# Kernel optimization log

Hardware: AMD Instinct MI355X
Metric: run time of the kernel (lower is better)

Reference implementation:

```python
import jax, jax.numpy as jnp
import numpy as np

NUM_HEADS = 8


def setup_inputs() -> dict:
    key = jax.random.key(0)
    ks = jax.random.split(key, 6)
    B, S, H = 2, 4096, 512
    Q = jax.random.normal(ks[0], (B, S, H), dtype=jnp.float32)
    K = jax.random.normal(ks[1], (B, S, H), dtype=jnp.float32)
    V = jax.random.normal(ks[2], (B, S, H), dtype=jnp.float32)
    risk_sigma = jax.random.uniform(ks[3], (B, 1), dtype=jnp.float32) * 0.2
    risk_lambda = jnp.array([2.0], dtype=jnp.float32)
    W_out = jax.random.normal(ks[4], (H, H), dtype=jnp.float32) * (1.0 / np.sqrt(H))
    b_out = jnp.zeros((H,), dtype=jnp.float32)
    return {"Q": Q, "K": K, "V": V, "risk_sigma": risk_sigma,
            "risk_lambda": risk_lambda, "W_out": W_out, "b_out": b_out}


def reference(Q, K, V, risk_sigma, risk_lambda, W_out, b_out):
    B, S, H = Q.shape
    nh = NUM_HEADS
    hd = H // nh
    # split heads: [B, S, nh, hd]
    q = Q.reshape(B, S, nh, hd)
    k = K.reshape(B, S, nh, hd)
    v = V.reshape(B, S, nh, hd)
    scale = 1.0 / jnp.sqrt(jnp.asarray(hd, dtype=Q.dtype))
    # [B, nh, S, S]
    scores = jnp.einsum('bshd,bthd->bhst', q, k) * scale
    # distance-based risk penalty
    pos = jnp.arange(S, dtype=Q.dtype)
    norm_dist = jnp.abs(pos[None, :] - pos[:, None]) / S  # [S, S]
    dist_sq = norm_dist ** 2
    sigma_c = jnp.clip(risk_sigma, 0.001, 0.2)            # [B, 1]
    sigma_n = (sigma_c - 0.001) / (0.2 - 0.001)
    lam = (risk_lambda / 10.0).reshape(())                 # scalar
    risk_term = lam * sigma_n[:, :, None, None] * dist_sq[None, None]  # [B,1,S,S]
    attn = jax.nn.softmax(scores - risk_term, axis=-1)
    ctx = jnp.einsum('bhst,bthd->bshd', attn, v).reshape(B, S, H)
    return ctx @ W_out.T + b_out
```

## Files before the change

kernel.cpp:

```cpp
#include <hip/hip_runtime.h>
#include <hip/hip_bf16.h>


#define S_LEN 4096
#define NHEAD 8
#define HD 64
#define HTOT 512

typedef __attribute__((ext_vector_type(8))) short short8;
typedef __attribute__((ext_vector_type(4))) float floatx4;
typedef __attribute__((ext_vector_type(2))) _Float16 half2v;

#if __has_builtin(__builtin_amdgcn_exp2f)
#define EXP2F(x) __builtin_amdgcn_exp2f(x)
#else
#define EXP2F(x) exp2f(x)
#endif

__device__ __forceinline__ unsigned pack_bf16(float a, float b) {
    unsigned ua = __builtin_bit_cast(unsigned, a) + 0x8000u;
    unsigned ub = __builtin_bit_cast(unsigned, b) + 0x8000u;
    return __builtin_amdgcn_perm(ub, ua, 0x07060302u);
}

__device__ __forceinline__ unsigned short f2bf(float x) {
    unsigned u = __builtin_bit_cast(unsigned, x) + 0x8000u;
    return (unsigned short)(u >> 16);
}

__device__ __forceinline__ void async16(const unsigned short* g, unsigned short* l) {
    __builtin_amdgcn_global_load_lds(
        (const __attribute__((address_space(1))) unsigned int*)g,
        (__attribute__((address_space(3))) unsigned int*)l, 16, 0, 0);
}

__global__ __launch_bounds__(256) void prep_kernel(
    const float* __restrict__ K, unsigned short* __restrict__ K16,
    const float* __restrict__ V, unsigned short* __restrict__ Vt,
    const float* __restrict__ W, unsigned short* __restrict__ W16)
{
    const int tid = threadIdx.x;
    if (blockIdx.x >= 3072) {
        size_t i = ((size_t)(blockIdx.x - 3072) * 256 + tid) * 8;
        float4 a = *(const float4*)(W + i);
        float4 b = *(const float4*)(W + i + 4);
        unsigned o[4] = {pack_bf16(a.x, a.y), pack_bf16(a.z, a.w),
                         pack_bf16(b.x, b.y), pack_bf16(b.z, b.w)};
        *(short8*)(W16 + i) = *(short8*)o;
    } else if (blockIdx.x < 2048) {
        size_t i = ((size_t)blockIdx.x * 256 + tid) * 8;
        float4 a = *(const float4*)(K + i);
        float4 b = *(const float4*)(K + i + 4);
        unsigned o[4] = {pack_bf16(a.x, a.y), pack_bf16(a.z, a.w),
                         pack_bf16(b.x, b.y), pack_bf16(b.z, b.w)};
        *(short8*)(K16 + i) = *(short8*)o;
    } else {
        __shared__ unsigned short T[64 * 66];
        const int blk = blockIdx.x - 2048;
        const int st = blk & 63;
        const int bh = blk >> 6;
        const int b = bh >> 3, h = bh & 7;
        const float* src = V + ((size_t)b * S_LEN + st * 64) * HTOT + h * HD;
        for (int i = 0; i < 4; i++) {
            int idx = tid + i * 256;
            int s = idx >> 4, c4 = idx & 15;
            float4 v = *(const float4*)(src + (size_t)s * HTOT + c4 * 4);
            T[(c4 * 4 + 0) * 66 + s] = f2bf(v.x);
            T[(c4 * 4 + 1) * 66 + s] = f2bf(v.y);
            T[(c4 * 4 + 2) * 66 + s] = f2bf(v.z);
            T[(c4 * 4 + 3) * 66 + s] = f2bf(v.w);
        }
        __syncthreads();
        unsigned short* dst = Vt + ((size_t)bh * 64) * S_LEN + st * 64;
        for (int i = 0; i < 2; i++) {
            int idx = tid + i * 256;
            int d = idx >> 3, c8 = idx & 7;
            uint2 lo = *(const uint2*)&T[d * 66 + c8 * 8];
            uint2 hi = *(const uint2*)&T[d * 66 + c8 * 8 + 4];
            unsigned o[4] = {lo.x, lo.y, hi.x, hi.y};
            *(short8*)(dst + (size_t)d * S_LEN + c8 * 8) = *(short8*)o;
        }
    }
}

__global__ __launch_bounds__(256, 4) void attn_kernel(
    const float* __restrict__ Q, const unsigned short* __restrict__ K16,
    const unsigned short* __restrict__ Vt,
    const float* __restrict__ risk_sigma, const float* __restrict__ risk_lambda,
    _Float16* __restrict__ Cpart, float* __restrict__ Lpart)
{
    __shared__ unsigned short Ksh[2][64 * 64];
    __shared__ unsigned short Vsh[2][64 * 64];

    const int tid  = threadIdx.x;
    const int wave = tid >> 6;
    const int lane = tid & 63;
    const int quad = lane >> 4;
    const int ln   = lane & 15;
    const int sw   = ln & 7;

    const int bid = blockIdx.x;
    const int ks  = bid & 1;
    const int qt  = (bid >> 1) & 31;
    const int h   = (bid >> 6) & 7;
    const int b   = bid >> 9;
    const int qbase = qt * 128;

    float sig = risk_sigma[b];
    sig = fminf(fmaxf(sig, 0.001f), 0.2f);
    const float sn   = (sig - 0.001f) * (1.0f / 0.199f);
    const float coef = risk_lambda[0] * 0.1f * sn;
    const float nc2 = -coef * (1.0f / 4096.0f) * (1.0f / 4096.0f) * 1.4426950408889634f;
    const float qscale = 0.125f * 1.4426950408889634f;

    const float* Qb = Q + (size_t)b * S_LEN * HTOT + (size_t)h * HD;
    const unsigned short* Kb = K16 + (size_t)b * S_LEN * HTOT + (size_t)h * HD;
    const unsigned short* Vb = Vt + ((size_t)(b * 8 + h) * 64) * S_LEN;

    const int rl  = lane >> 3;
    const int c8g = ((lane & 7) ^ rl) << 3;
    const int ksrow = ((wave & 1) << 4) | (((rl >> 2) & 1) << 3)
                    | ((wave >> 1) << 2) | (rl & 3);

    auto dma = [&](int buf, int kb) {
        const unsigned short* gv = Vb + (size_t)(wave * 8 + rl) * S_LEN + kb + c8g;
        async16(Kb + (size_t)(kb + ksrow) * HTOT + c8g,
                &Ksh[buf][wave * 512 + lane * 8]);
        async16(Kb + (size_t)(kb + 32 + ksrow) * HTOT + c8g,
                &Ksh[buf][(wave + 4) * 512 + lane * 8]);
        async16(gv,              &Vsh[buf][wave * 512 + lane * 8]);
        async16(gv + 32 * S_LEN, &Vsh[buf][(wave + 4) * 512 + lane * 8]);
    };

    dma(0, ks * 2048);

    short8 qf[2][2];
    {
        const float* qp0 = Qb + (size_t)(qbase + wave * 32 + ln) * HTOT + quad * 8;
        #pragma unroll
        for (int nt = 0; nt < 2; nt++) {
            const float* qp = qp0 + (size_t)(nt * 16) * HTOT;
            #pragma unroll
            for (int half = 0; half < 2; half++) {
                float4 x = *(const float4*)(qp + half * 32);
                float4 y = *(const float4*)(qp + half * 32 + 4);
                unsigned o[4] = {pack_bf16(x.x * qscale, x.y * qscale),
                                 pack_bf16(x.z * qscale, x.w * qscale),
                                 pack_bf16(y.x * qscale, y.y * qscale),
                                 pack_bf16(y.z * qscale, y.w * qscale)};
                qf[nt][half] = *(short8*)o;
            }
        }
    }
    __syncthreads();

    const short sone = (short)0x3F80;
    const short8 ones = {sone, sone, sone, sone, sone, sone, sone, sone};

    floatx4 Oacc[2][4], Lacc[2];
    #pragma unroll
    for (int nt = 0; nt < 2; nt++) {
        Lacc[nt] = (floatx4){0.f, 0.f, 0.f, 0.f};
        #pragma unroll
        for (int dt = 0; dt < 4; dt++) Oacc[nt][dt] = (floatx4){0.f, 0.f, 0.f, 0.f};
    }

    const int qa = qbase + wave * 32;
    const float quad8f = (float)(quad * 8);

    for (int kt = 0; kt < 32; ++kt) {
        const int kbase = ks * 2048 + kt * 64;
        const int cur = kt & 1;
        if (kt < 31) dma(1 - cur, kbase + 64);
        const unsigned short* Kc = Ksh[cur];
        const unsigned short* Vc = Vsh[cur];

        const float dqq = (float)(qa + ln - kbase) - quad8f;
        unsigned pw[2][2][4];

        #pragma unroll
        for (int jt = 0; jt < 4; jt++) {
            const int krow = (jt * 16 + ln) * 64;
            short8 ak0 = *(const short8*)&Kc[krow + ((quad ^ sw) << 3)];
            short8 ak1 = *(const short8*)&Kc[krow + (((quad + 4) ^ sw) << 3)];
            const float jtoff = (float)((jt >> 1) * 32 + (jt & 1) * 4);
            #pragma unroll
            for (int nt = 0; nt < 2; nt++) {
                float d = dqq + ((float)(nt * 16) - jtoff);
                floatx4 rk;
                #pragma unroll
                for (int r = 0; r < 4; r++) {
                    rk[r] = (nc2 * d) * d;
                    d -= 1.0f;
                }
                floatx4 s = __builtin_amdgcn_mfma_f32_16x16x32_bf16(ak0, qf[nt][0], rk, 0, 0, 0);
                s = __builtin_amdgcn_mfma_f32_16x16x32_bf16(ak1, qf[nt][1], s, 0, 0, 0);
                float p0 = EXP2F(s[0]);
                float p1 = EXP2F(s[1]);
                float p2 = EXP2F(s[2]);
                float p3 = EXP2F(s[3]);
                pw[nt][jt >> 1][(jt & 1) * 2 + 0] = pack_bf16(p0, p1);
                pw[nt][jt >> 1][(jt & 1) * 2 + 1] = pack_bf16(p2, p3);
            }
        }

        __builtin_amdgcn_s_setprio(1);
        #pragma unroll
        for (int dt = 0; dt < 4; dt++) {
            const int vrow = (dt * 16 + ln) * 64;
            short8 bv0 = *(const short8*)&Vc[vrow + ((quad ^ sw) << 3)];
            short8 bv1 = *(const short8*)&Vc[vrow + (((quad + 4) ^ sw) << 3)];
            #pragma unroll
            for (int nt = 0; nt < 2; nt++) {
                short8 pa0 = *(const short8*)&pw[nt][0][0];
                short8 pa1 = *(const short8*)&pw[nt][1][0];
                Oacc[nt][dt] = __builtin_amdgcn_mfma_f32_16x16x32_bf16(pa0, bv0, Oacc[nt][dt], 0, 0, 0);
                Oacc[nt][dt] = __builtin_amdgcn_mfma_f32_16x16x32_bf16(pa1, bv1, Oacc[nt][dt], 0, 0, 0);
            }
        }
        #pragma unroll
        for (int nt = 0; nt < 2; nt++) {
            short8 pa0 = *(const short8*)&pw[nt][0][0];
            short8 pa1 = *(const short8*)&pw[nt][1][0];
            Lacc[nt] = __builtin_amdgcn_mfma_f32_16x16x32_bf16(pa0, ones, Lacc[nt], 0, 0, 0);
            Lacc[nt] = __builtin_amdgcn_mfma_f32_16x16x32_bf16(pa1, ones, Lacc[nt], 0, 0, 0);
        }
        __builtin_amdgcn_s_setprio(0);
        __syncthreads();
    }

    _Float16* Cw = Cpart + (size_t)bid * (128 * 64);
    for (int nt = 0; nt < 2; nt++) {
        if (ln == 0) {
            #pragma unroll
            for (int r = 0; r < 4; r++)
                Lpart[bid * 128 + wave * 32 + nt * 16 + quad * 4 + r] = Lacc[nt][r];
        }
        float rl4[4];
        #pragma unroll
        for (int r = 0; r < 4; r++) rl4[r] = 1.0f / Lacc[nt][r];
        for (int dt = 0; dt < 4; dt++)
            #pragma unroll
            for (int r = 0; r < 4; r++) {
                int q = wave * 32 + nt * 16 + quad * 4 + r;
                Cw[q * 64 + dt * 16 + ln] = (_Float16)(Oacc[nt][dt][r] * rl4[r]);
            }
    }
}

__global__ __launch_bounds__(256) void combine_kernel(
    const _Float16* __restrict__ Cpart, const float* __restrict__ Lpart,
    unsigned short* __restrict__ ctx)
{
    const int t = threadIdx.x;
    const int tile = blockIdx.x;
    const int qt = tile & 31, h = (tile >> 5) & 7, b = tile >> 8;
    __shared__ float w0s[128], w1s[128];
    if (t < 128) {
        float l0 = Lpart[(tile * 2 + 0) * 128 + t];
        float l1 = Lpart[(tile * 2 + 1) * 128 + t];
        float inv = 1.0f / (l0 + l1);
        w0s[t] = l0 * inv;
        w1s[t] = l1 * inv;
    }
    __syncthreads();
    const _Float16* C0 = Cpart + (size_t)(tile * 2) * (128 * 64);
    const _Float16* C1 = C0 + 128 * 64;
    for (int i = 0; i < 8; i++) {
        int e = (i * 256 + t) * 4;
        int q = e >> 6, d = e & 63;
        half2v a0 = *(const half2v*)(C0 + e);
        half2v a1 = *(const half2v*)(C0 + e + 2);
        half2v b0 = *(const half2v*)(C1 + e);
        half2v b1 = *(const half2v*)(C1 + e + 2);
        float w0 = w0s[q], w1 = w1s[q];
        float v0 = w0 * (float)a0[0] + w1 * (float)b0[0];
        float v1 = w0 * (float)a0[1] + w1 * (float)b0[1];
        float v2 = w0 * (float)a1[0] + w1 * (float)b1[0];
        float v3 = w0 * (float)a1[1] + w1 * (float)b1[1];
        uint2 o;
        o.x = pack_bf16(v0, v1);
        o.y = pack_bf16(v2, v3);
        *(uint2*)&ctx[((size_t)b * S_LEN + qt * 128 + q) * HTOT + h * HD + d] = o;
    }
}

__global__ __launch_bounds__(256) void proj_kernel(
    const unsigned short* __restrict__ A,
    const unsigned short* __restrict__ W16,
    const float* __restrict__ bias,
    float* __restrict__ out)
{
    __shared__ unsigned short Ash[2][64 * 32];
    __shared__ unsigned short Bsh[2][128 * 32];
    const int tid = threadIdx.x;
    const int wave = tid >> 6, lane = tid & 63, quad = lane >> 4, ln = lane & 15;
    const int wr = wave >> 1, wc = wave & 1;
    const int m0 = blockIdx.y * 64;
    const int nb = blockIdx.x * 128;

    const int arow = (wave * 64 + lane) >> 2;
    const int ac   = (wave * 64 + lane) & 3;
    const int acs  = (ac ^ ((arow >> 1) & 3)) << 3;
    const int wrow0 = (wave * 64 + lane) >> 2;
    const int wc0   = (wave * 64 + lane) & 3;
    const int wcs0  = (wc0 ^ ((wrow0 >> 1) & 3)) << 3;
    const int wrow1 = wrow0 + 64;
    const int wcs1  = (wc0 ^ ((wrow1 >> 1) & 3)) << 3;

    auto dma = [&](int buf, int k0) {
        async16(A + (size_t)(m0 + arow) * 512 + k0 + acs,
                &Ash[buf][wave * 512 + lane * 8]);
        async16(W16 + (size_t)(nb + wrow0) * 512 + k0 + wcs0,
                &Bsh[buf][wave * 512 + lane * 8]);
        async16(W16 + (size_t)(nb + wrow1) * 512 + k0 + wcs1,
                &Bsh[buf][(wave + 4) * 512 + lane * 8]);
    };

    floatx4 acc[2][4];
    for (int i = 0; i < 2; i++)
        for (int j = 0; j < 4; j++) acc[i][j] = (floatx4){0.f, 0.f, 0.f, 0.f};

    dma(0, 0);
    for (int kt = 0; kt < 16; ++kt) {
        const int cur = kt & 1;
        __syncthreads();
        if (kt < 15) dma(1 - cur, (kt + 1) * 32);

        short8 af[2], bf[4];
        for (int i = 0; i < 2; i++) {
            int r = wr * 32 + i * 16 + ln;
            af[i] = *(const short8*)&Ash[cur][r * 32 + ((quad ^ ((r >> 1) & 3)) << 3)];
        }
        for (int j = 0; j < 4; j++) {
            int r = wc * 64 + j * 16 + ln;
            bf[j] = *(const short8*)&Bsh[cur][r * 32 + ((quad ^ ((r >> 1) & 3)) << 3)];
        }
        for (int i = 0; i < 2; i++)
            for (int j = 0; j < 4; j++)
                acc[i][j] = __builtin_amdgcn_mfma_f32_16x16x32_bf16(af[i], bf[j], acc[i][j], 0, 0, 0);
    }

    for (int i = 0; i < 2; i++) {
        int row = m0 + wr * 32 + i * 16 + quad * 4;
        for (int j = 0; j < 4; j++) {
            int col = nb + wc * 64 + j * 16 + ln;
            float bv = bias[col];
            #pragma unroll
            for (int r = 0; r < 4; r++)
                out[(size_t)(row + r) * 512 + col] = acc[i][j][r] + bv;
        }
    }
}

extern "C" void kernel_launch(void* const* d_in, const int* in_sizes, int n_in,
                              void* d_out, int out_size, void* d_ws, size_t ws_size,
                              hipStream_t stream) {
    const float* Q    = (const float*)d_in[0];
    const float* K    = (const float*)d_in[1];
    const float* V    = (const float*)d_in[2];
    const float* sig  = (const float*)d_in[3];
    const float* lam  = (const float*)d_in[4];
    const float* W    = (const float*)d_in[5];
    const float* bias = (const float*)d_in[6];

    unsigned short* K16 = (unsigned short*)d_ws;
    unsigned short* Vt  = (unsigned short*)((char*)d_ws + (8u << 20));
    unsigned short* ctx = (unsigned short*)((char*)d_ws + (16u << 20));
    float* Lpart        = (float*)((char*)d_ws + (24u << 20));
    unsigned short* W16 = (unsigned short*)((char*)d_ws + (24u << 20) + (512u << 10));
    _Float16* Cpart     = (_Float16*)d_out;
    float* out = (float*)d_out;

    prep_kernel<<<dim3(3200), dim3(256), 0, stream>>>(K, K16, V, Vt, W, W16);
    attn_kernel<<<dim3(1024), dim3(256), 0, stream>>>(Q, K16, Vt, sig, lam, Cpart, Lpart);
    combine_kernel<<<dim3(512), dim3(256), 0, stream>>>(Cpart, Lpart, ctx);
    proj_kernel<<<dim3(4, 128), dim3(256), 0, stream>>>(ctx, W16, bias, out);
}
```

Baseline: 205.8 us.

## Fuse split-K combine into attention block using two wave groups

After: 201.3 us. -2.2%, faster.

```diff
diff --git a/kernel.cpp b/kernel.cpp
--- a/kernel.cpp
+++ b/kernel.cpp
@@ -9,7 +9,6 @@
 
 typedef __attribute__((ext_vector_type(8))) short short8;
 typedef __attribute__((ext_vector_type(4))) float floatx4;
-typedef __attribute__((ext_vector_type(2))) _Float16 half2v;
 
 #if __has_builtin(__builtin_amdgcn_exp2f)
 #define EXP2F(x) __builtin_amdgcn_exp2f(x)
@@ -83,27 +82,27 @@
     }
 }
 
-__global__ __launch_bounds__(256, 4) void attn_kernel(
+__global__ __launch_bounds__(512, 4) void attn_kernel(
     const float* __restrict__ Q, const unsigned short* __restrict__ K16,
     const unsigned short* __restrict__ Vt,
     const float* __restrict__ risk_sigma, const float* __restrict__ risk_lambda,
-    _Float16* __restrict__ Cpart, float* __restrict__ Lpart)
+    unsigned short* __restrict__ ctx)
 {
-    __shared__ unsigned short Ksh[2][64 * 64];
-    __shared__ unsigned short Vsh[2][64 * 64];
+    __shared__ unsigned short SH[32768];
 
     const int tid  = threadIdx.x;
     const int wave = tid >> 6;
+    const int grp  = wave >> 2;
+    const int wv   = wave & 3;
     const int lane = tid & 63;
     const int quad = lane >> 4;
     const int ln   = lane & 15;
     const int sw   = ln & 7;
 
     const int bid = blockIdx.x;
-    const int ks  = bid & 1;
-    const int qt  = (bid >> 1) & 31;
-    const int h   = (bid >> 6) & 7;
-    const int b   = bid >> 9;
+    const int qt  = bid & 31;
+    const int h   = (bid >> 5) & 7;
+    const int b   = bid >> 8;
     const int qbase = qt * 128;
 
     float sig = risk_sigma[b];
@@ -119,24 +118,25 @@
 
     const int rl  = lane >> 3;
     const int c8g = ((lane & 7) ^ rl) << 3;
-    const int ksrow = ((wave & 1) << 4) | (((rl >> 2) & 1) << 3)
-                    | ((wave >> 1) << 2) | (rl & 3);
+    const int ksrow = ((wv & 1) << 4) | (((rl >> 2) & 1) << 3)
+                    | ((wv >> 1) << 2) | (rl & 3);
 
     auto dma = [&](int buf, int kb) {
-        const unsigned short* gv = Vb + (size_t)(wave * 8 + rl) * S_LEN + kb + c8g;
-        async16(Kb + (size_t)(kb + ksrow) * HTOT + c8g,
-                &Ksh[buf][wave * 512 + lane * 8]);
-        async16(Kb + (size_t)(kb + 32 + ksrow) * HTOT + c8g,
-                &Ksh[buf][(wave + 4) * 512 + lane * 8]);
-        async16(gv,              &Vsh[buf][wave * 512 + lane * 8]);
-        async16(gv + 32 * S_LEN, &Vsh[buf][(wave + 4) * 512 + lane * 8]);
+        unsigned short* base = SH + (grp * 2 + buf) * 8192;
+        const unsigned short* gk = Kb + (size_t)(kb + ksrow) * HTOT + c8g;
+        const unsigned short* gv = Vb + (size_t)(wv * 8 + rl) * S_LEN + kb + c8g;
+        async16(gk,              base + wv * 512 + lane * 8);
+        async16(gk + 32 * HTOT,  base + (wv + 4) * 512 + lane * 8);
+        async16(gv,              base + 4096 + wv * 512 + lane * 8);
+        async16(gv + 32 * S_LEN, base + 4096 + (wv + 4) * 512 + lane * 8);
     };
 
-    dma(0, ks * 2048);
+    const int kb0 = grp * 2048;
+    dma(0, kb0);
 
     short8 qf[2][2];
     {
-        const float* qp0 = Qb + (size_t)(qbase + wave * 32 + ln) * HTOT + quad * 8;
+        const float* qp0 = Qb + (size_t)(qbase + wv * 32 + ln) * HTOT + quad * 8;
         #pragma unroll
         for (int nt = 0; nt < 2; nt++) {
             const float* qp = qp0 + (size_t)(nt * 16) * HTOT;
@@ -165,15 +165,15 @@
         for (int dt = 0; dt < 4; dt++) Oacc[nt][dt] = (floatx4){0.f, 0.f, 0.f, 0.f};
     }
 
-    const int qa = qbase + wave * 32;
+    const int qa = qbase + wv * 32;
     const float quad8f = (float)(quad * 8);
 
     for (int kt = 0; kt < 32; ++kt) {
-        const int kbase = ks * 2048 + kt * 64;
+        const int kbase = kb0 + kt * 64;
         const int cur = kt & 1;
         if (kt < 31) dma(1 - cur, kbase + 64);
-        const unsigned short* Kc = Ksh[cur];
-        const unsigned short* Vc = Vsh[cur];
+        const unsigned short* Kc = SH + (grp * 2 + cur) * 8192;
+        const unsigned short* Vc = Kc + 4096;
 
         const float dqq = (float)(qa + ln - kbase) - quad8f;
         unsigned pw[2][2][4];
@@ -229,59 +229,61 @@
         __syncthreads();
     }
 
-    _Float16* Cw = Cpart + (size_t)bid * (128 * 64);
-    for (int nt = 0; nt < 2; nt++) {
-        if (ln == 0) {
+    float* X   = (float*)SH;
+    float* Lsh = (float*)SH + 128 * 68;
+
+    if (ln == 0) {
+        #pragma unroll
+        for (int nt = 0; nt < 2; nt++)
             #pragma unroll
             for (int r = 0; r < 4; r++)
-                Lpart[bid * 128 + wave * 32 + nt * 16 + quad * 4 + r] = Lacc[nt][r];
-        }
-        float rl4[4];
-        #pragma unroll
-        for (int r = 0; r < 4; r++) rl4[r] = 1.0f / Lacc[nt][r];
-        for (int dt = 0; dt < 4; dt++)
+                Lsh[grp * 128 + wv * 32 + nt * 16 + quad * 4 + r] = Lacc[nt][r];
+    }
+    if (grp == 0) {
+        #pragma unroll
+        for (int nt = 0; nt < 2; nt++)
+            #pragma unroll
+            for (int dt = 0; dt < 4; dt++)
+                #pragma unroll
+                for (int r = 0; r < 4; r++)
+                    X[(wv * 32 + nt * 16 + quad * 4 + r) * 68 + dt * 16 + ln] = Oacc[nt][dt][r];
+    }
+    __syncthreads();
+    if (grp == 1) {
+        #pragma unroll
+        for (int nt = 0; nt < 2; nt++) {
+            float inv[4];
             #pragma unroll
             for (int r = 0; r < 4; r++) {
-                int q = wave * 32 + nt * 16 + quad * 4 + r;
-                Cw[q * 64 + dt * 16 + ln] = (_Float16)(Oacc[nt][dt][r] * rl4[r]);
+                int row = wv * 32 + nt * 16 + quad * 4 + r;
+                inv[r] = 1.0f / (Lsh[row] + Lsh[128 + row]);
             }
-    }
-}
-
-__global__ __launch_bounds__(256) void combine_kernel(
-    const _Float16* __restrict__ Cpart, const float* __restrict__ Lpart,
-    unsigned short* __restrict__ ctx)
-{
-    const int t = threadIdx.x;
-    const int tile = blockIdx.x;
-    const int qt = tile & 31, h = (tile >> 5) & 7, b = tile >> 8;
-    __shared__ float w0s[128], w1s[128];
-    if (t < 128) {
-        float l0 = Lpart[(tile * 2 + 0) * 128 + t];
-        float l1 = Lpart[(tile * 2 + 1) * 128 + t];
-        float inv = 1.0f / (l0 + l1);
-        w0s[t] = l0 * inv;
-        w1s[t] = l1 * inv;
+            #pragma unroll
+            for (int dt = 0; dt < 4; dt++)
+                #pragma unroll
+                for (int r = 0; r < 4; r++) {
+                    int row = wv * 32 + nt * 16 + quad * 4 + r;
+                    float* p = &X[row * 68 + dt * 16 + ln];
+                    *p = (*p + Oacc[nt][dt][r]) * inv[r];
+                }
+        }
     }
     __syncthreads();
-    const _Float16* C0 = Cpart + (size_t)(tile * 2) * (128 * 64);
-    const _Float16* C1 = C0 + 128 * 64;
-    for (int i = 0; i < 8; i++) {
-        int e = (i * 256 + t) * 4;
-        int q = e >> 6, d = e & 63;
-        half2v a0 = *(const half2v*)(C0 + e);
-        half2v a1 = *(const half2v*)(C0 + e + 2);
-        half2v b0 = *(const half2v*)(C1 + e);
-        half2v b1 = *(const half2v*)(C1 + e + 2);
-        float w0 = w0s[q], w1 = w1s[q];
-        float v0 = w0 * (float)a0[0] + w1 * (float)b0[0];
-        float v1 = w0 * (float)a0[1] + w1 * (float)b0[1];
-        float v2 = w0 * (float)a1[0] + w1 * (float)b1[0];
-        float v3 = w0 * (float)a1[1] + w1 * (float)b1[1];
-        uint2 o;
-        o.x = pack_bf16(v0, v1);
-        o.y = pack_bf16(v2, v3);
-        *(uint2*)&ctx[((size_t)b * S_LEN + qt * 128 + q) * HTOT + h * HD + d] = o;
+    {
+        const int q = tid >> 2;
+        const int c = tid & 3;
+        const float* xp = X + q * 68 + c * 16;
+        float4 x0 = *(const float4*)(xp + 0);
+        float4 x1 = *(const float4*)(xp + 4);
+        float4 x2 = *(const float4*)(xp + 8);
+        float4 x3 = *(const float4*)(xp + 12);
+        unsigned o0[4] = {pack_bf16(x0.x, x0.y), pack_bf16(x0.z, x0.w),
+                          pack_bf16(x1.x, x1.y), pack_bf16(x1.z, x1.w)};
+        unsigned o1[4] = {pack_bf16(x2.x, x2.y), pack_bf16(x2.z, x2.w),
+                          pack_bf16(x3.x, x3.y), pack_bf16(x3.z, x3.w)};
+        unsigned short* cp = ctx + ((size_t)b * S_LEN + qbase + q) * HTOT + h * HD + c * 16;
+        *(short8*)cp       = *(short8*)o0;
+        *(short8*)(cp + 8) = *(short8*)o1;
     }
 }
 
@@ -367,13 +369,10 @@
     unsigned short* K16 = (unsigned short*)d_ws;
     unsigned short* Vt  = (unsigned short*)((char*)d_ws + (8u << 20));
     unsigned short* ctx = (unsigned short*)((char*)d_ws + (16u << 20));
-    float* Lpart        = (float*)((char*)d_ws + (24u << 20));
-    unsigned short* W16 = (unsigned short*)((char*)d_ws + (24u << 20) + (512u << 10));
-    _Float16* Cpart     = (_Float16*)d_out;
+    unsigned short* W16 = (unsigned short*)((char*)d_ws + (24u << 20));
     float* out = (float*)d_out;
 
     prep_kernel<<<dim3(3200), dim3(256), 0, stream>>>(K, K16, V, Vt, W, W16);
-    attn_kernel<<<dim3(1024), dim3(256), 0, stream>>>(Q, K16, Vt, sig, lam, Cpart, Lpart);
-    combine_kernel<<<dim3(512), dim3(256), 0, stream>>>(Cpart, Lpart, ctx);
+    attn_kernel<<<dim3(512), dim3(512), 0, stream>>>(Q, K16, Vt, sig, lam, ctx);
     proj_kernel<<<dim3(4, 128), dim3(256), 0, stream>>>(ctx, W16, bias, out);
 }
```
